# Performance work log

Measured on AMD Instinct MI355X. Metric: run time of the kernel, lower is better.

The kernel has to match this reference:

```python
import jax, jax.numpy as jnp
import numpy as np

B, S, D = 2, 2048, 1024
H = 16
DH = D // H  # 64


def setup_inputs() -> dict:
    key = jax.random.key(0)
    k1, k2, k3 = jax.random.split(key, 3)
    X = jax.random.normal(k1, (B, S, D), dtype=jnp.float32)
    # xavier_normal for Linear(D, 3*D): std = sqrt(2/(fan_in+fan_out))
    std_qkv = float(np.sqrt(2.0 / (D + 3 * D)))
    std_out = float(np.sqrt(2.0 / (D + D)))
    W_qkv = jax.random.normal(k2, (3 * H * DH, D), dtype=jnp.float32) * std_qkv
    W_out = jax.random.normal(k3, (D, H * DH), dtype=jnp.float32) * std_out
    return {"X": X, "W_qkv": W_qkv, "W_out": W_out}


def reference(X, W_qkv, W_out):
    b, s, d = X.shape
    # stacked projection: (b, s, 3*H*DH), then per-head chunk into q,k,v
    qkv = jnp.einsum('bsd,ed->bse', X, W_qkv)
    qkv = qkv.reshape(b, s, H, 3 * DH)
    q, k, v = jnp.split(qkv, 3, axis=-1)  # each (b, s, H, DH)
    scale = 1.0 / jnp.sqrt(jnp.asarray(DH, dtype=X.dtype))
    # naive unfused attention: full [b,H,s,s] score matrix
    scores = jnp.einsum('bqhd,bkhd->bhqk', q, k) * scale
    attn = jax.nn.softmax(scores, axis=-1)
    vals = jnp.einsum('bhqk,bkhd->bqhd', attn, v)
    vals = vals.reshape(b, s, H * DH)
    out = jnp.einsum('bse,de->bsd', vals, W_out)
    return out
```

## Files before the change

kernel.cpp:

```cpp
#include <hip/hip_runtime.h>
#include <cstdint>
#include <cstddef>

typedef __bf16 bf16;
typedef __bf16 bf16x8 __attribute__((ext_vector_type(8)));
typedef __bf16 bf16x2 __attribute__((ext_vector_type(2)));
typedef float  floatx4 __attribute__((ext_vector_type(4)));
typedef unsigned uintx4 __attribute__((ext_vector_type(4)));

typedef __attribute__((address_space(1))) void gvoid_t;
typedef __attribute__((address_space(3))) void lvoid_t;

#define MFMA16(a, b, c) __builtin_amdgcn_mfma_f32_16x16x32_bf16((a), (b), (c), 0, 0, 0)

#if __has_builtin(__builtin_amdgcn_exp2f)
#define EXP2(x) __builtin_amdgcn_exp2f(x)
#else
#define EXP2(x) exp2f(x)
#endif

#define S_TOK 2048
#define E3 3072
#define DMODEL 1024

#define NX 4194304
#define NWQ 3145728
#define NWO 1048576
__global__ __launch_bounds__(256) void cvt_all(const float* __restrict__ X,
                                               const float* __restrict__ Wq,
                                               const float* __restrict__ Wo,
                                               bf16* __restrict__ Xb,
                                               bf16* __restrict__ Wqb,
                                               bf16* __restrict__ Wob) {
  int i = (blockIdx.x * 256 + threadIdx.x) * 8;
  const float* s;
  bf16* d;
  float sc = 1.0f;
  int off;
  if (i < NX) {
    s = X; d = Xb; off = i;
  } else if (i < NX + NWQ) {
    off = i - NX; s = Wq; d = Wqb;
    int row = off >> 10;
    if ((row % 192) < 64) sc = 0.18033688011f;
  } else {
    off = i - NX - NWQ; s = Wo; d = Wob;
  }
  const float4* p = (const float4*)(s + off);
  float4 a = p[0], b = p[1];
  bf16x8 o;
  o[0] = (bf16)(a.x * sc); o[1] = (bf16)(a.y * sc);
  o[2] = (bf16)(a.z * sc); o[3] = (bf16)(a.w * sc);
  o[4] = (bf16)(b.x * sc); o[5] = (bf16)(b.y * sc);
  o[6] = (bf16)(b.z * sc); o[7] = (bf16)(b.w * sc);
  *(bf16x8*)(d + off) = o;
}

__device__ __forceinline__ void gl_lds16(const bf16* g, bf16* l) {
  __builtin_amdgcn_global_load_lds((gvoid_t*)g, (lvoid_t*)l, 16, 0, 0);
}

template <bool OUT_BF16, bool FUSE_V>
__global__ __launch_bounds__(256) void gemm_bt(const bf16* __restrict__ A,
                                               const bf16* __restrict__ Bt,
                                               void* __restrict__ Cv,
                                               bf16* __restrict__ Vt,
                                               int M, int N, int K) {
  __shared__ bf16 sA[128 * 64];
  __shared__ bf16 sB[128 * 64];
  const int tid = threadIdx.x;
  const int wv = tid >> 6, lane = tid & 63;
  const int wr = wv >> 1, wc = wv & 1;
  const int lrow = lane & 15, lgrp = lane >> 4;
  const int R0 = blockIdx.y * 128, C0 = blockIdx.x * 128;

  floatx4 acc[4][4] = {};

  const int srow = lane >> 3;
  const int schk = (lane & 7) ^ srow;
  const bf16* gA = A + (size_t)(R0 + wv * 32 + srow) * K + schk * 8;
  const bf16* gB = Bt + (size_t)(C0 + wv * 32 + srow) * K + schk * 8;
  bf16* lA = sA + wv * 32 * 64;
  bf16* lB = sB + wv * 32 * 64;
  const size_t rs8 = (size_t)8 * K;

  for (int k0 = 0; k0 < K; k0 += 64) {
#pragma unroll
    for (int c = 0; c < 4; c++) {
      gl_lds16(gA + k0 + c * rs8, lA + c * 512);
      gl_lds16(gB + k0 + c * rs8, lB + c * 512);
    }
    __syncthreads();
#pragma unroll
    for (int kk = 0; kk < 2; kk++) {
      bf16x8 af[4], bfr[4];
#pragma unroll
      for (int i = 0; i < 4; i++) {
        int r = wr * 64 + i * 16 + lrow;
        af[i] = *(const bf16x8*)&sA[r * 64 + ((kk * 4 + lgrp) ^ (r & 7)) * 8];
      }
#pragma unroll
      for (int j = 0; j < 4; j++) {
        int r = wc * 64 + j * 16 + lrow;
        bfr[j] = *(const bf16x8*)&sB[r * 64 + ((kk * 4 + lgrp) ^ (r & 7)) * 8];
      }
#pragma unroll
      for (int i = 0; i < 4; i++)
#pragma unroll
        for (int j = 0; j < 4; j++)
          acc[i][j] = MFMA16(af[i], bfr[j], acc[i][j]);
    }
    __syncthreads();
  }

  const int rbase = R0 + wr * 64 + lgrp * 4;
  const int cbase = C0 + wc * 64 + lrow;
  if (OUT_BF16) {
    bf16* C = (bf16*)Cv;
#pragma unroll
    for (int i = 0; i < 4; i++)
#pragma unroll
      for (int j = 0; j < 4; j++) {
        const int col = cbase + j * 16;
        const int m192 = col % 192;
        const int hh = col / 192;
#pragma unroll
        for (int r = 0; r < 4; r++) {
          const int row = rbase + i * 16 + r;
          bf16 val = (bf16)acc[i][j][r];
          bf16* dst;
          if (FUSE_V && m192 >= 128) {
            const int sl = row & 2047;
            const int sl5 = sl & 31;
            const int q5 = (((sl5 >> 2) & 3) << 3) | (((sl5 >> 4) & 1) << 2) | (sl5 & 3);
            const int sp = (sl & ~31) | q5;
            dst = Vt + ((size_t)(((row >> 11) * 16 + hh) * 64 + (m192 - 128))) * S_TOK + sp;
          } else {
            dst = C + (size_t)row * N + col;
          }
          *dst = val;
        }
      }
  } else {
    float* C = (float*)Cv;
#pragma unroll
    for (int i = 0; i < 4; i++)
#pragma unroll
      for (int j = 0; j < 4; j++)
#pragma unroll
        for (int r = 0; r < 4; r++)
          C[(size_t)(rbase + i * 16 + r) * N + cbase + j * 16] = acc[i][j][r];
  }
}

__global__ __launch_bounds__(256) void gemm_bt_n64(const bf16* __restrict__ A,
                                                   const bf16* __restrict__ Bt,
                                                   float* __restrict__ C,
                                                   int M, int N, int K) {
  __shared__ bf16 sA[128 * 64];
  __shared__ bf16 sB[64 * 64];
  const int tid = threadIdx.x;
  const int wv = tid >> 6, lane = tid & 63;
  const int wr = wv >> 1, wc = wv & 1;
  const int lrow = lane & 15, lgrp = lane >> 4;
  const int R0 = blockIdx.y * 128, C0 = blockIdx.x * 64;

  floatx4 acc[4][2] = {};

  const int srow = lane >> 3;
  const int schk = (lane & 7) ^ srow;
  const bf16* gA = A + (size_t)(R0 + wv * 32 + srow) * K + schk * 8;
  const bf16* gB = Bt + (size_t)(C0 + wv * 16 + srow) * K + schk * 8;
  bf16* lA = sA + wv * 32 * 64;
  bf16* lB = sB + wv * 16 * 64;
  const size_t rs8 = (size_t)8 * K;

  for (int k0 = 0; k0 < K; k0 += 64) {
#pragma unroll
    for (int c = 0; c < 4; c++) gl_lds16(gA + k0 + c * rs8, lA + c * 512);
#pragma unroll
    for (int c = 0; c < 2; c++) gl_lds16(gB + k0 + c * rs8, lB + c * 512);
    __syncthreads();
#pragma unroll
    for (int kk = 0; kk < 2; kk++) {
      bf16x8 af[4], bfr[2];
#pragma unroll
      for (int i = 0; i < 4; i++) {
        int r = wr * 64 + i * 16 + lrow;
        af[i] = *(const bf16x8*)&sA[r * 64 + ((kk * 4 + lgrp) ^ (r & 7)) * 8];
      }
#pragma unroll
      for (int j = 0; j < 2; j++) {
        int r = wc * 32 + j * 16 + lrow;
        bfr[j] = *(const bf16x8*)&sB[r * 64 + ((kk * 4 + lgrp) ^ (r & 7)) * 8];
      }
#pragma unroll
      for (int i = 0; i < 4; i++)
#pragma unroll
        for (int j = 0; j < 2; j++)
          acc[i][j] = MFMA16(af[i], bfr[j], acc[i][j]);
    }
    __syncthreads();
  }

  const int rbase = R0 + wr * 64 + lgrp * 4;
  const int cbase = C0 + wc * 32 + lrow;
#pragma unroll
  for (int i = 0; i < 4; i++)
#pragma unroll
    for (int j = 0; j < 2; j++)
#pragma unroll
      for (int r = 0; r < 4; r++)
        C[(size_t)(rbase + i * 16 + r) * N + cbase + j * 16] = acc[i][j][r];
}

__global__ __launch_bounds__(512, 2) void attn(const bf16* __restrict__ qkv,
                                               const bf16* __restrict__ Vt,
                                               bf16* __restrict__ vals) {
  __shared__ bf16 sK[2][128 * 64];
  __shared__ bf16 sV[2][64 * 128];

  const int tid = threadIdx.x;
  const int wv = tid >> 6, lane = tid & 63;
  const int lrow = lane & 15, lgrp = lane >> 4;
  const int b = blockIdx.z, h = blockIdx.x;
  const int qb = blockIdx.y * 256;

  const int srow = lane >> 3;
  const int scol = (lane & 7) ^ srow;
  const bf16* kg0 = qkv + (size_t)(b * S_TOK + wv * 8 + srow) * E3 + h * 192 + 64 + scol * 8;
  const int vrow = lane >> 4;
  const int vchk = lane & 15;
  const int d0 = wv * 8 + vrow, d1 = d0 + 4;
  const bf16* vg0 = Vt + (size_t)((b * 16 + h) * 64 + d0) * S_TOK + (vchk ^ (d0 & 15)) * 8;
  const bf16* vg1 = Vt + (size_t)((b * 16 + h) * 64 + d1) * S_TOK + (vchk ^ (d1 & 15)) * 8;

  const bf16* qp = qkv + (size_t)(b * S_TOK + qb + wv * 32) * E3 + h * 192;
  bf16x8 qa[2][2];
#pragma unroll
  for (int rt = 0; rt < 2; rt++)
#pragma unroll
    for (int dh = 0; dh < 2; dh++)
      qa[rt][dh] = *(const bf16x8*)(qp + (size_t)(rt * 16 + lrow) * E3 + dh * 32 + lgrp * 8);

  floatx4 O[2][4] = {};
  float lsum[2] = {0.f, 0.f};

  auto stage = [&](int buf, int st) {
    const bf16* kg = kg0 + (size_t)st * 128 * E3;
    gl_lds16(kg, &sK[buf][wv * 512]);
    gl_lds16(kg + (size_t)64 * E3, &sK[buf][4096 + wv * 512]);
    gl_lds16(vg0 + st * 128, &sV[buf][wv * 1024]);
    gl_lds16(vg1 + st * 128, &sV[buf][wv * 1024 + 512]);
  };

  auto qk_g = [&](int buf, int g, floatx4 (&sc)[2][2]) {
    bf16x8 kf[2][2];
#pragma unroll
    for (int t = 0; t < 2; t++)
#pragma unroll
      for (int dh = 0; dh < 2; dh++)
        kf[t][dh] = *(const bf16x8*)&sK[buf][(g * 32 + t * 16 + lrow) * 64 +
                                            ((dh * 4 + lgrp) ^ (lrow & 7)) * 8];
    __builtin_amdgcn_s_setprio(1);
#pragma unroll
    for (int rt = 0; rt < 2; rt++) {
      floatx4 a0 = {0.f, 0.f, 0.f, 0.f}, a1 = {0.f, 0.f, 0.f, 0.f};
      a0 = MFMA16(kf[0][0], qa[rt][0], a0);
      a0 = MFMA16(kf[0][1], qa[rt][1], a0);
      a1 = MFMA16(kf[1][0], qa[rt][0], a1);
      a1 = MFMA16(kf[1][1], qa[rt][1], a1);
      sc[rt][0] = a0;
      sc[rt][1] = a1;
    }
    __builtin_amdgcn_s_setprio(0);
  };

  auto sm_g = [&](floatx4 (&sc)[2][2], unsigned (&pfw)[2][4]) {
#pragma unroll
    for (int rt = 0; rt < 2; rt++) {
      float e0 = EXP2(sc[rt][0][0]), e1 = EXP2(sc[rt][0][1]);
      float e2 = EXP2(sc[rt][0][2]), e3 = EXP2(sc[rt][0][3]);
      float e4 = EXP2(sc[rt][1][0]), e5 = EXP2(sc[rt][1][1]);
      float e6 = EXP2(sc[rt][1][2]), e7 = EXP2(sc[rt][1][3]);
      lsum[rt] += ((e0 + e1) + (e2 + e3)) + ((e4 + e5) + (e6 + e7));
      bf16x2 w;
      w[0] = (bf16)e0; w[1] = (bf16)e1;
      pfw[rt][0] = __builtin_bit_cast(unsigned, w);
      w[0] = (bf16)e2; w[1] = (bf16)e3;
      pfw[rt][1] = __builtin_bit_cast(unsigned, w);
      w[0] = (bf16)e4; w[1] = (bf16)e5;
      pfw[rt][2] = __builtin_bit_cast(unsigned, w);
      w[0] = (bf16)e6; w[1] = (bf16)e7;
      pfw[rt][3] = __builtin_bit_cast(unsigned, w);
    }
  };

  auto pv_g = [&](int buf, int g, unsigned (&pfw)[2][4]) {
    bf16x8 vf[4];
#pragma unroll
    for (int dt = 0; dt < 4; dt++)
      vf[dt] = *(const bf16x8*)&sV[buf][(dt * 16 + lrow) * 128 + ((g * 4 + lgrp) ^ lrow) * 8];
    __builtin_amdgcn_s_setprio(1);
#pragma unroll
    for (int rt = 0; rt < 2; rt++) {
      uintx4 pw = {pfw[rt][0], pfw[rt][1], pfw[rt][2], pfw[rt][3]};
      bf16x8 pf = __builtin_bit_cast(bf16x8, pw);
#pragma unroll
      for (int dt = 0; dt < 4; dt++) O[rt][dt] = MFMA16(pf, vf[dt], O[rt][dt]);
    }
    __builtin_amdgcn_s_setprio(0);
  };

  auto compute = [&](int buf) {
    floatx4 scA[2][2], scB[2][2];
    unsigned pfA[2][4], pfB[2][4];
    qk_g(buf, 0, scA); sm_g(scA, pfA);
    qk_g(buf, 1, scB); sm_g(scB, pfB); pv_g(buf, 0, pfA);
    qk_g(buf, 2, scA); sm_g(scA, pfA); pv_g(buf, 1, pfB);
    qk_g(buf, 3, scB); sm_g(scB, pfB); pv_g(buf, 2, pfA);
    pv_g(buf, 3, pfB);
  };

  stage(0, 0);
  __syncthreads();
#pragma unroll 1
  for (int st = 0; st < 16; st += 2) {
    stage(1, st + 1);
    compute(0);
    __syncthreads();
    if (st + 2 < 16) stage(0, st + 2);
    compute(1);
    __syncthreads();
  }

#pragma unroll
  for (int rt = 0; rt < 2; rt++) {
    lsum[rt] += __shfl_xor(lsum[rt], 16);
    lsum[rt] += __shfl_xor(lsum[rt], 32);
  }

  bf16* vout = vals + (size_t)(b * S_TOK + qb + wv * 32) * DMODEL + h * 64;
#pragma unroll
  for (int rt = 0; rt < 2; rt++)
#pragma unroll
    for (int r = 0; r < 4; r++) {
      float rs = __shfl(lsum[rt], lgrp * 4 + r);
      float rinv = __builtin_amdgcn_rcpf(rs);
#pragma unroll
      for (int dt = 0; dt < 4; dt++)
        vout[(size_t)(rt * 16 + lgrp * 4 + r) * DMODEL + dt * 16 + lrow] =
            (bf16)(O[rt][dt][r] * rinv);
    }
}

extern "C" void kernel_launch(void* const* d_in, const int* in_sizes, int n_in,
                              void* d_out, int out_size, void* d_ws, size_t ws_size,
                              hipStream_t stream) {
  const float* X = (const float*)d_in[0];
  const float* Wqkv = (const float*)d_in[1];
  const float* Wout = (const float*)d_in[2];
  float* out = (float*)d_out;

  char* ws = (char*)d_ws;
  bf16* Xb = (bf16*)(ws);
  bf16* Wqb = (bf16*)(ws + ((size_t)8 << 20));
  bf16* Wob = (bf16*)(ws + ((size_t)14 << 20));
  bf16* qkvb = (bf16*)(ws + ((size_t)16 << 20));
  bf16* Vt = (bf16*)(ws + ((size_t)40 << 20));
  bf16* vals = (bf16*)(ws + ((size_t)48 << 20));

  cvt_all<<<(NX + NWQ + NWO) / 2048, 256, 0, stream>>>(X, Wqkv, Wout, Xb, Wqb, Wob);

  gemm_bt<true, true><<<dim3(24, 32), 256, 0, stream>>>(Xb, Wqb, qkvb, Vt, 4096, 3072, 1024);

  attn<<<dim3(16, 8, 2), 512, 0, stream>>>(qkvb, Vt, vals);

  gemm_bt_n64<<<dim3(16, 32), 256, 0, stream>>>(vals, Wob, out, 4096, 1024, 1024);
}
```

Measured before the change: 170.0 us.

## Split attention keys across wave pairs and write head-major Q/K layouts

```diff
diff --git a/kernel.cpp b/kernel.cpp
--- a/kernel.cpp
+++ b/kernel.cpp
@@ -4,6 +4,7 @@
 
 typedef __bf16 bf16;
 typedef __bf16 bf16x8 __attribute__((ext_vector_type(8)));
+typedef __bf16 bf16x4 __attribute__((ext_vector_type(4)));
 typedef __bf16 bf16x2 __attribute__((ext_vector_type(2)));
 typedef float  floatx4 __attribute__((ext_vector_type(4)));
 typedef unsigned uintx4 __attribute__((ext_vector_type(4)));
@@ -65,6 +66,7 @@
                                                const bf16* __restrict__ Bt,
                                                void* __restrict__ Cv,
                                                bf16* __restrict__ Vt,
+                                               bf16* __restrict__ Qt,
                                                int M, int N, int K) {
   __shared__ bf16 sA[128 * 64];
   __shared__ bf16 sB[128 * 64];
@@ -116,31 +118,50 @@
   const int rbase = R0 + wr * 64 + lgrp * 4;
   const int cbase = C0 + wc * 64 + lrow;
   if (OUT_BF16) {
-    bf16* C = (bf16*)Cv;
-#pragma unroll
-    for (int i = 0; i < 4; i++)
-#pragma unroll
-      for (int j = 0; j < 4; j++) {
-        const int col = cbase + j * 16;
-        const int m192 = col % 192;
-        const int hh = col / 192;
-#pragma unroll
-        for (int r = 0; r < 4; r++) {
-          const int row = rbase + i * 16 + r;
-          bf16 val = (bf16)acc[i][j][r];
-          bf16* dst;
-          if (FUSE_V && m192 >= 128) {
-            const int sl = row & 2047;
-            const int sl5 = sl & 31;
-            const int q5 = (((sl5 >> 2) & 3) << 3) | (((sl5 >> 4) & 1) << 2) | (sl5 & 3);
-            const int sp = (sl & ~31) | q5;
-            dst = Vt + ((size_t)(((row >> 11) * 16 + hh) * 64 + (m192 - 128))) * S_TOK + sp;
-          } else {
-            dst = C + (size_t)row * N + col;
-          }
-          *dst = val;
+    const int bb = R0 >> 11;
+    const int tokb0 = rbase & 2047;
+#pragma unroll
+    for (int j = 0; j < 4; j++) {
+      const int col = cbase + j * 16;
+      const int m192 = col % 192;
+      const int hh = col / 192;
+      if (FUSE_V && m192 < 64) {
+        bf16* qdst = Qt + (size_t)((bb * 16 + hh) * 64 + m192) * S_TOK + tokb0;
+#pragma unroll
+        for (int i = 0; i < 4; i++) {
+          bf16x4 v;
+          v[0] = (bf16)acc[i][j][0]; v[1] = (bf16)acc[i][j][1];
+          v[2] = (bf16)acc[i][j][2]; v[3] = (bf16)acc[i][j][3];
+          *(bf16x4*)(qdst + i * 16) = v;
         }
-      }
+      } else if (FUSE_V && m192 >= 128) {
+        bf16* vdst = Vt + (size_t)((bb * 16 + hh) * 64 + (m192 - 128)) * S_TOK;
+#pragma unroll
+        for (int i = 0; i < 4; i++) {
+          const int t0 = tokb0 + i * 16;
+          const int b5 = t0 & 31;
+          const int q5 = (((b5 >> 2) & 3) << 3) | (((b5 >> 4) & 1) << 2);
+          bf16x4 v;
+          v[0] = (bf16)acc[i][j][0]; v[1] = (bf16)acc[i][j][1];
+          v[2] = (bf16)acc[i][j][2]; v[3] = (bf16)acc[i][j][3];
+          *(bf16x4*)(vdst + ((t0 & ~31) | q5)) = v;
+        }
+      } else if (FUSE_V) {
+        bf16* kdst = (bf16*)Cv + ((size_t)((bb * 16 + hh) * 2048 + tokb0)) * 64 + (m192 - 64);
+#pragma unroll
+        for (int i = 0; i < 4; i++)
+#pragma unroll
+          for (int r = 0; r < 4; r++)
+            kdst[(size_t)(i * 16 + r) * 64] = (bf16)acc[i][j][r];
+      } else {
+        bf16* C = (bf16*)Cv;
+#pragma unroll
+        for (int i = 0; i < 4; i++)
+#pragma unroll
+          for (int r = 0; r < 4; r++)
+            C[(size_t)(rbase + i * 16 + r) * N + col] = (bf16)acc[i][j][r];
+      }
+    }
   } else {
     float* C = (float*)Cv;
 #pragma unroll
@@ -214,8 +235,9 @@
         C[(size_t)(rbase + i * 16 + r) * N + cbase + j * 16] = acc[i][j][r];
 }
 
-__global__ __launch_bounds__(512, 2) void attn(const bf16* __restrict__ qkv,
+__global__ __launch_bounds__(512, 4) void attn(const bf16* __restrict__ Kc,
                                                const bf16* __restrict__ Vt,
+                                               const bf16* __restrict__ Qt,
                                                bf16* __restrict__ vals) {
   __shared__ bf16 sK[2][128 * 64];
   __shared__ bf16 sV[2][64 * 128];
@@ -223,38 +245,43 @@
   const int tid = threadIdx.x;
   const int wv = tid >> 6, lane = tid & 63;
   const int lrow = lane & 15, lgrp = lane >> 4;
+  const int wq = wv >> 1, wk = wv & 1;
   const int b = blockIdx.z, h = blockIdx.x;
-  const int qb = blockIdx.y * 256;
+  const int qb = blockIdx.y * 128;
 
   const int srow = lane >> 3;
   const int scol = (lane & 7) ^ srow;
-  const bf16* kg0 = qkv + (size_t)(b * S_TOK + wv * 8 + srow) * E3 + h * 192 + 64 + scol * 8;
+  const bf16* kg0 = Kc + (size_t)((b * 16 + h) * 2048 + wv * 8 + srow) * 64 + scol * 8;
   const int vrow = lane >> 4;
   const int vchk = lane & 15;
   const int d0 = wv * 8 + vrow, d1 = d0 + 4;
   const bf16* vg0 = Vt + (size_t)((b * 16 + h) * 64 + d0) * S_TOK + (vchk ^ (d0 & 15)) * 8;
   const bf16* vg1 = Vt + (size_t)((b * 16 + h) * 64 + d1) * S_TOK + (vchk ^ (d1 & 15)) * 8;
 
-  const bf16* qp = qkv + (size_t)(b * S_TOK + qb + wv * 32) * E3 + h * 192;
+  const bf16* qtp = Qt + (size_t)((b * 16 + h) * 64) * S_TOK + (qb + wq * 32 + lrow);
   bf16x8 qa[2][2];
 #pragma unroll
   for (int rt = 0; rt < 2; rt++)
 #pragma unroll
     for (int dh = 0; dh < 2; dh++)
-      qa[rt][dh] = *(const bf16x8*)(qp + (size_t)(rt * 16 + lrow) * E3 + dh * 32 + lgrp * 8);
+#pragma unroll
+      for (int j = 0; j < 8; j++)
+        qa[rt][dh][j] = qtp[(size_t)(dh * 32 + lgrp * 8 + j) * S_TOK + rt * 16];
 
   floatx4 O[2][4] = {};
   float lsum[2] = {0.f, 0.f};
+  const int gbase = wk * 2;
 
   auto stage = [&](int buf, int st) {
-    const bf16* kg = kg0 + (size_t)st * 128 * E3;
+    const bf16* kg = kg0 + (size_t)st * 128 * 64;
     gl_lds16(kg, &sK[buf][wv * 512]);
-    gl_lds16(kg + (size_t)64 * E3, &sK[buf][4096 + wv * 512]);
+    gl_lds16(kg + 64 * 64, &sK[buf][4096 + wv * 512]);
     gl_lds16(vg0 + st * 128, &sV[buf][wv * 1024]);
     gl_lds16(vg1 + st * 128, &sV[buf][wv * 1024 + 512]);
   };
 
-  auto qk_g = [&](int buf, int g, floatx4 (&sc)[2][2]) {
+  auto qk_g = [&](int buf, int gg, floatx4 (&sc)[2][2]) {
+    const int g = gbase + gg;
     bf16x8 kf[2][2];
 #pragma unroll
     for (int t = 0; t < 2; t++)
@@ -296,7 +323,8 @@
     }
   };
 
-  auto pv_g = [&](int buf, int g, unsigned (&pfw)[2][4]) {
+  auto pv_g = [&](int buf, int gg, unsigned (&pfw)[2][4]) {
+    const int g = gbase + gg;
     bf16x8 vf[4];
 #pragma unroll
     for (int dt = 0; dt < 4; dt++)
@@ -316,10 +344,9 @@
     floatx4 scA[2][2], scB[2][2];
     unsigned pfA[2][4], pfB[2][4];
     qk_g(buf, 0, scA); sm_g(scA, pfA);
-    qk_g(buf, 1, scB); sm_g(scB, pfB); pv_g(buf, 0, pfA);
-    qk_g(buf, 2, scA); sm_g(scA, pfA); pv_g(buf, 1, pfB);
-    qk_g(buf, 3, scB); sm_g(scB, pfB); pv_g(buf, 2, pfA);
-    pv_g(buf, 3, pfB);
+    qk_g(buf, 1, scB); sm_g(scB, pfB);
+    pv_g(buf, 0, pfA);
+    pv_g(buf, 1, pfB);
   };
 
   stage(0, 0);
@@ -340,18 +367,41 @@
     lsum[rt] += __shfl_xor(lsum[rt], 32);
   }
 
-  bf16* vout = vals + (size_t)(b * S_TOK + qb + wv * 32) * DMODEL + h * 64;
-#pragma unroll
-  for (int rt = 0; rt < 2; rt++)
-#pragma unroll
-    for (int r = 0; r < 4; r++) {
-      float rs = __shfl(lsum[rt], lgrp * 4 + r);
-      float rinv = __builtin_amdgcn_rcpf(rs);
-#pragma unroll
-      for (int dt = 0; dt < 4; dt++)
-        vout[(size_t)(rt * 16 + lgrp * 4 + r) * DMODEL + dt * 16 + lrow] =
-            (bf16)(O[rt][dt][r] * rinv);
-    }
+  float* s0 = (float*)&sK[0][0];
+  float* s1 = (float*)&sV[0][0];
+  const int sidx = (wq * 64 + lane) * 20;
+  if (wk == 1) {
+#pragma unroll
+    for (int dt = 0; dt < 4; dt++) {
+      *(floatx4*)&s0[sidx + dt * 4] = O[0][dt];
+      *(floatx4*)&s1[sidx + dt * 4] = O[1][dt];
+    }
+    s0[sidx + 16] = lsum[0];
+    s1[sidx + 16] = lsum[1];
+  }
+  __syncthreads();
+  if (wk == 0) {
+#pragma unroll
+    for (int dt = 0; dt < 4; dt++) {
+      O[0][dt] += *(const floatx4*)&s0[sidx + dt * 4];
+      O[1][dt] += *(const floatx4*)&s1[sidx + dt * 4];
+    }
+    lsum[0] += s0[sidx + 16];
+    lsum[1] += s1[sidx + 16];
+
+    bf16* vout = vals + (size_t)(b * S_TOK + qb + wq * 32) * DMODEL + h * 64;
+#pragma unroll
+    for (int rt = 0; rt < 2; rt++)
+#pragma unroll
+      for (int r = 0; r < 4; r++) {
+        float rs = __shfl(lsum[rt], lgrp * 4 + r);
+        float rinv = __builtin_amdgcn_rcpf(rs);
+#pragma unroll
+        for (int dt = 0; dt < 4; dt++)
+          vout[(size_t)(rt * 16 + lgrp * 4 + r) * DMODEL + dt * 16 + lrow] =
+              (bf16)(O[rt][dt][r] * rinv);
+      }
+  }
 }
 
 extern "C" void kernel_launch(void* const* d_in, const int* in_sizes, int n_in,
@@ -366,15 +416,16 @@
   bf16* Xb = (bf16*)(ws);
   bf16* Wqb = (bf16*)(ws + ((size_t)8 << 20));
   bf16* Wob = (bf16*)(ws + ((size_t)14 << 20));
-  bf16* qkvb = (bf16*)(ws + ((size_t)16 << 20));
-  bf16* Vt = (bf16*)(ws + ((size_t)40 << 20));
-  bf16* vals = (bf16*)(ws + ((size_t)48 << 20));
+  bf16* Kc = (bf16*)(ws + ((size_t)16 << 20));
+  bf16* Vt = (bf16*)(ws + ((size_t)24 << 20));
+  bf16* Qt = (bf16*)(ws + ((size_t)32 << 20));
+  bf16* vals = (bf16*)(ws + ((size_t)40 << 20));
 
   cvt_all<<<(NX + NWQ + NWO) / 2048, 256, 0, stream>>>(X, Wqkv, Wout, Xb, Wqb, Wob);
 
-  gemm_bt<true, true><<<dim3(24, 32), 256, 0, stream>>>(Xb, Wqb, qkvb, Vt, 4096, 3072, 1024);
-
-  attn<<<dim3(16, 8, 2), 512, 0, stream>>>(qkvb, Vt, vals);
+  gemm_bt<true, true><<<dim3(24, 32), 256, 0, stream>>>(Xb, Wqb, Kc, Vt, Qt, 4096, 3072, 1024);
+
+  attn<<<dim3(16, 16, 2), 512, 0, stream>>>(Kc, Vt, Qt, vals);
 
   gemm_bt_n64<<<dim3(16, 32), 256, 0, stream>>>(vals, Wob, out, 4096, 1024, 1024);
 }
```

New measurement: 174.2 us. 1.03x slower.
